# Optimization experiments

Measured on AMD Instinct MI355X. Metric: run time of the kernel, lower is better.

The kernel has to match this reference:

```python
import jax, jax.numpy as jnp
import numpy as np

BINS = 30
MOMENTUM = 0.75
LOSS_WEIGHT = 1.0


def setup_inputs() -> dict:
    key = jax.random.key(0)
    k1, k2 = jax.random.split(key)
    N, C = 8192, 2048
    preds = jax.random.normal(k1, (N, C), dtype=jnp.float32)
    targets = jax.random.randint(k2, (N, C), 0, 2).astype(jnp.int32)  # binary multi-hot
    acc_sum = jnp.zeros((BINS, C), dtype=jnp.float32)  # EMA histogram state
    return {"preds": preds, "targets": targets, "acc_sum": acc_sum}


def reference(preds, targets, acc_sum):
    N, C = preds.shape
    t = targets.astype(preds.dtype)

    # gradient norm g = |sigmoid(p) - t|, detached (weights carry no grad)
    g = jnp.abs(jax.nn.sigmoid(jax.lax.stop_gradient(preds)) - t)

    # bin index: edges[i] = i/BINS, so bin = floor(g*BINS), g=1.0 -> last bin (edge[-1]+=1e-6)
    bin_idx = jnp.clip(jnp.floor(g * BINS).astype(jnp.int32), 0, BINS - 1)  # [N, C]

    # per-label histogram: counts[b, c] = #examples with bin b in column c
    cols = jnp.broadcast_to(jnp.arange(C, dtype=jnp.int32)[None, :], (N, C))
    counts = jnp.zeros((BINS, C), dtype=preds.dtype).at[bin_idx, cols].add(1.0)

    # n[c] = number of non-empty bins for label c
    n = jnp.sum(counts >= 1.0, axis=0).astype(preds.dtype)  # [C]

    # EMA update of the histogram (momentum > 0 branch)
    acc_new = MOMENTUM * acc_sum + (1.0 - MOMENTUM) * counts  # [BINS, C]

    tot = jnp.asarray(float(max(N, 1.0)), preds.dtype)
    weights = tot / acc_new[bin_idx, cols]               # gather per-element density
    weights = weights / jnp.maximum(n, 1.0)[None, :]      # normalize by #valid bins
    weights = jax.lax.stop_gradient(weights)

    # BCE with logits, elementwise: softplus-style stable form
    bce = jnp.logaddexp(0.0, preds) - preds * t
    loss = jnp.mean(weights * bce)
    return loss * LOSS_WEIGHT
```

## Files before the change

### kernel.cpp

```cpp
#include <hip/hip_runtime.h>

#define BINS  30
#define NROWS 8192
#define NCOLS 2048
#define COLS_PER_BLK 256
#define ROWS_PER_BLK 128
#define YSLICES 64

#define FIXED_SCALE 16384.0f
#define CNT_SHIFT   24
#define SUM_MASK    ((1u << CNT_SHIFT) - 1)

#define WS_PART  0
#define WS_CNT   (YSLICES * BINS * NCOLS * 4)
#define WS_BSUM  (WS_CNT + BINS * NCOLS * 4)
#define WS_BPART (WS_BSUM + BINS * NCOLS * 4)

__global__ __launch_bounds__(1024, 8) void k_main(
    const float* __restrict__ preds, const int* __restrict__ targets,
    unsigned int* __restrict__ part)
{
    __shared__ unsigned int h[BINS * COLS_PER_BLK];
    const int tid = threadIdx.x;
    for (int i = tid; i < BINS * COLS_PER_BLK; i += 1024) h[i] = 0u;
    __syncthreads();

    const int wave = tid >> 6;
    const int lane = tid & 63;
    const int colBase = blockIdx.x * COLS_PER_BLK;
    const int col0 = colBase + 4 * lane;
    const int r0   = blockIdx.y * ROWS_PER_BLK + wave * 8;

    const float4* P = (const float4*)(preds   + (size_t)r0 * NCOLS + col0);
    const int4*   T = (const int4*)  (targets + (size_t)r0 * NCOLS + col0);
    const int RV = NCOLS / 4;

    float4 pc0 = P[0], pc1 = P[RV];
    int4   tc0 = T[0], tc1 = T[RV];

    #pragma unroll
    for (int q = 0; q < 4; ++q) {
        float4 pn0, pn1;
        int4   tn0, tn1;
        if (q < 3) {
            P += 2 * RV; T += 2 * RV;
            pn0 = P[0]; pn1 = P[RV];
            tn0 = T[0]; tn1 = T[RV];
        }
        __builtin_amdgcn_sched_barrier(0);

        const float4 pb[2] = {pc0, pc1};
        const int4   tb[2] = {tc0, tc1};
        #pragma unroll
        for (int r = 0; r < 2; ++r) {
            const float pv[4] = {pb[r].x, pb[r].y, pb[r].z, pb[r].w};
            const int   tv[4] = {tb[r].x, tb[r].y, tb[r].z, tb[r].w};
            #pragma unroll
            for (int j = 0; j < 4; ++j) {
                float p  = pv[j];
                float pp = tv[j] ? -p : p;
                float e  = __expf(-fabsf(pp));
                float d  = 1.0f + e;
                float r1 = __builtin_amdgcn_rcpf(d);
                float g  = (pp >= 0.0f) ? r1 : e * r1;
                int   b  = (int)(g * 30.0f);
                b = b > (BINS - 1) ? (BINS - 1) : b;
                float bce = fmaxf(pp, 0.0f) + __logf(d);
                unsigned int pk = (1u << CNT_SHIFT)
                    | (unsigned int)(bce * FIXED_SCALE + 0.5f);
                atomicAdd(&h[b * COLS_PER_BLK + (j << 6) + lane], pk);
            }
        }
        pc0 = pn0; pc1 = pn1;
        tc0 = tn0; tc1 = tn1;
    }
    __syncthreads();

    const size_t outBase = (size_t)blockIdx.y * BINS * NCOLS + colBase;
    for (int i = tid; i < BINS * COLS_PER_BLK; i += 1024) {
        const int b = i >> 8;
        const int r = i & 255;
        const int l = r >> 2;
        const int j = r & 3;
        part[outBase + (size_t)b * NCOLS + r] = h[b * COLS_PER_BLK + (j << 6) + l];
    }
}

__global__ __launch_bounds__(256) void k_reduce(
    const unsigned int* __restrict__ part,
    float* __restrict__ cnt_f, float* __restrict__ bsum_f)
{
    const int id = blockIdx.x * 256 + threadIdx.x;
    unsigned int cnt = 0u, sm = 0u;
    #pragma unroll 16
    for (int y = 0; y < YSLICES; ++y) {
        const unsigned int v = part[(size_t)y * BINS * NCOLS + id];
        cnt += v >> CNT_SHIFT;
        sm  += v & SUM_MASK;
    }
    cnt_f[id]  = (float)cnt;
    bsum_f[id] = (float)sm * (1.0f / FIXED_SCALE);
}

__global__ __launch_bounds__(256) void k_colsum(
    const float* __restrict__ cnt_f, const float* __restrict__ bsum_f,
    const float* __restrict__ acc_sum, float* __restrict__ blockPart)
{
    __shared__ float wave_sums[4];
    const int tid = threadIdx.x;
    const int c   = blockIdx.x * 256 + tid;

    float colsum = 0.0f;
    int n = 0;
    #pragma unroll
    for (int b = 0; b < BINS; ++b) {
        const size_t gidx = (size_t)b * NCOLS + c;
        const float cnt = cnt_f[gidx];
        if (cnt >= 1.0f) {
            n += 1;
            float acc_new = 0.75f * acc_sum[gidx] + 0.25f * cnt;
            colsum += bsum_f[gidx] / acc_new;
        }
    }
    colsum /= (float)((n > 1 ? n : 1) * NCOLS);

    #pragma unroll
    for (int off = 32; off > 0; off >>= 1)
        colsum += __shfl_down(colsum, off, 64);
    if ((tid & 63) == 0) wave_sums[tid >> 6] = colsum;
    __syncthreads();
    if (tid == 0)
        blockPart[blockIdx.x] = wave_sums[0] + wave_sums[1] + wave_sums[2] + wave_sums[3];
}

__global__ void k_final(const float* __restrict__ blockPart, float* __restrict__ out)
{
    double s = 0.0;
    #pragma unroll
    for (int i = 0; i < 8; ++i) s += (double)blockPart[i];
    out[0] = (float)s;
}

extern "C" void kernel_launch(void* const* d_in, const int* in_sizes, int n_in,
                              void* d_out, int out_size, void* d_ws, size_t ws_size,
                              hipStream_t stream)
{
    const float* preds   = (const float*)d_in[0];
    const int*   targets = (const int*)d_in[1];
    const float* acc_sum = (const float*)d_in[2];

    unsigned int* part = (unsigned int*)((char*)d_ws + WS_PART);
    float* cnt_f       = (float*)((char*)d_ws + WS_CNT);
    float* bsum_f      = (float*)((char*)d_ws + WS_BSUM);
    float* blockPart   = (float*)((char*)d_ws + WS_BPART);

    dim3 gA(NCOLS / COLS_PER_BLK, NROWS / ROWS_PER_BLK);
    k_main<<<gA, 1024, 0, stream>>>(preds, targets, part);

    k_reduce<<<(BINS * NCOLS) / 256, 256, 0, stream>>>(part, cnt_f, bsum_f);

    k_colsum<<<NCOLS / 256, 256, 0, stream>>>(cnt_f, bsum_f, acc_sum, blockPart);

    k_final<<<1, 1, 0, stream>>>(blockPart, (float*)d_out);
}
```

Baseline: 179.6 us.

## Replace LDS atomic histogram with per-thread register histograms per column

Each thread now owns a single column and accumulates its 30-bin packed count/sum histogram in registers using unrolled compare-select adds, instead of shared-memory atomics. This removes the LDS atomic traffic and the shared-memory init and flush. The block shape changes to 512 threads covering 512 columns, and the target sign flip becomes an XOR. In exchange it adds 30 VALU ops per element, uses more registers, loads narrower scalar data instead of float4, and launches fewer waves.

```diff
diff --git a/kernel.cpp b/kernel.cpp
--- a/kernel.cpp
+++ b/kernel.cpp
@@ -3,10 +3,8 @@
 #define BINS  30
 #define NROWS 8192
 #define NCOLS 2048
-#define COLS_PER_BLK 256
+#define YSLICES 64
 #define ROWS_PER_BLK 128
-#define YSLICES 64
-
 #define FIXED_SCALE 16384.0f
 #define CNT_SHIFT   24
 #define SUM_MASK    ((1u << CNT_SHIFT) - 1)
@@ -16,74 +14,62 @@
 #define WS_BSUM  (WS_CNT + BINS * NCOLS * 4)
 #define WS_BPART (WS_BSUM + BINS * NCOLS * 4)
 
-__global__ __launch_bounds__(1024, 8) void k_main(
+__device__ __forceinline__ void accum(float p, int t, unsigned int (&h)[BINS])
+{
+    float pp = __int_as_float(__float_as_int(p) ^ (t << 31));
+    float e  = __expf(-fabsf(pp));
+    float d  = 1.0f + e;
+    float r1 = __builtin_amdgcn_rcpf(d);
+    float g  = (pp >= 0.0f) ? r1 : e * r1;
+    int   b  = (int)(g * 30.0f);
+    b = b > (BINS - 1) ? (BINS - 1) : b;
+    float bce = fmaxf(pp, 0.0f) + __logf(d);
+    unsigned int pk = (1u << CNT_SHIFT)
+        | (unsigned int)(bce * FIXED_SCALE + 0.5f);
+    #pragma unroll
+    for (int bb = 0; bb < BINS; ++bb)
+        h[bb] += (b == bb) ? pk : 0u;
+}
+
+__global__ __launch_bounds__(512, 4) void k_main(
     const float* __restrict__ preds, const int* __restrict__ targets,
     unsigned int* __restrict__ part)
 {
-    __shared__ unsigned int h[BINS * COLS_PER_BLK];
     const int tid = threadIdx.x;
-    for (int i = tid; i < BINS * COLS_PER_BLK; i += 1024) h[i] = 0u;
-    __syncthreads();
+    const int col = blockIdx.x * 512 + tid;
+    const int r0  = blockIdx.y * ROWS_PER_BLK;
 
-    const int wave = tid >> 6;
-    const int lane = tid & 63;
-    const int colBase = blockIdx.x * COLS_PER_BLK;
-    const int col0 = colBase + 4 * lane;
-    const int r0   = blockIdx.y * ROWS_PER_BLK + wave * 8;
+    unsigned int h[BINS];
+    #pragma unroll
+    for (int b = 0; b < BINS; ++b) h[b] = 0u;
 
-    const float4* P = (const float4*)(preds   + (size_t)r0 * NCOLS + col0);
-    const int4*   T = (const int4*)  (targets + (size_t)r0 * NCOLS + col0);
-    const int RV = NCOLS / 4;
+    const float* P = preds   + (size_t)r0 * NCOLS + col;
+    const int*   T = targets + (size_t)r0 * NCOLS + col;
 
-    float4 pc0 = P[0], pc1 = P[RV];
-    int4   tc0 = T[0], tc1 = T[RV];
+    float pc[4]; int tc[4];
+    #pragma unroll
+    for (int i = 0; i < 4; ++i) { pc[i] = P[i * NCOLS]; tc[i] = T[i * NCOLS]; }
 
-    #pragma unroll
-    for (int q = 0; q < 4; ++q) {
-        float4 pn0, pn1;
-        int4   tn0, tn1;
-        if (q < 3) {
-            P += 2 * RV; T += 2 * RV;
-            pn0 = P[0]; pn1 = P[RV];
-            tn0 = T[0]; tn1 = T[RV];
+    for (int batch = 0; batch < ROWS_PER_BLK / 4; ++batch) {
+        float pn[4]; int tn[4];
+        if (batch < ROWS_PER_BLK / 4 - 1) {
+            P += 4 * NCOLS; T += 4 * NCOLS;
+            #pragma unroll
+            for (int i = 0; i < 4; ++i) { pn[i] = P[i * NCOLS]; tn[i] = T[i * NCOLS]; }
         }
         __builtin_amdgcn_sched_barrier(0);
 
-        const float4 pb[2] = {pc0, pc1};
-        const int4   tb[2] = {tc0, tc1};
         #pragma unroll
-        for (int r = 0; r < 2; ++r) {
-            const float pv[4] = {pb[r].x, pb[r].y, pb[r].z, pb[r].w};
-            const int   tv[4] = {tb[r].x, tb[r].y, tb[r].z, tb[r].w};
-            #pragma unroll
-            for (int j = 0; j < 4; ++j) {
-                float p  = pv[j];
-                float pp = tv[j] ? -p : p;
-                float e  = __expf(-fabsf(pp));
-                float d  = 1.0f + e;
-                float r1 = __builtin_amdgcn_rcpf(d);
-                float g  = (pp >= 0.0f) ? r1 : e * r1;
-                int   b  = (int)(g * 30.0f);
-                b = b > (BINS - 1) ? (BINS - 1) : b;
-                float bce = fmaxf(pp, 0.0f) + __logf(d);
-                unsigned int pk = (1u << CNT_SHIFT)
-                    | (unsigned int)(bce * FIXED_SCALE + 0.5f);
-                atomicAdd(&h[b * COLS_PER_BLK + (j << 6) + lane], pk);
-            }
-        }
-        pc0 = pn0; pc1 = pn1;
-        tc0 = tn0; tc1 = tn1;
+        for (int i = 0; i < 4; ++i) accum(pc[i], tc[i], h);
+
+        #pragma unroll
+        for (int i = 0; i < 4; ++i) { pc[i] = pn[i]; tc[i] = tn[i]; }
     }
-    __syncthreads();
 
-    const size_t outBase = (size_t)blockIdx.y * BINS * NCOLS + colBase;
-    for (int i = tid; i < BINS * COLS_PER_BLK; i += 1024) {
-        const int b = i >> 8;
-        const int r = i & 255;
-        const int l = r >> 2;
-        const int j = r & 3;
-        part[outBase + (size_t)b * NCOLS + r] = h[b * COLS_PER_BLK + (j << 6) + l];
-    }
+    unsigned int* base = part + (size_t)blockIdx.y * BINS * NCOLS + col;
+    #pragma unroll
+    for (int b = 0; b < BINS; ++b)
+        base[(size_t)b * NCOLS] = h[b];
 }
 
 __global__ __launch_bounds__(256) void k_reduce(
@@ -154,8 +140,8 @@
     float* bsum_f      = (float*)((char*)d_ws + WS_BSUM);
     float* blockPart   = (float*)((char*)d_ws + WS_BPART);
 
-    dim3 gA(NCOLS / COLS_PER_BLK, NROWS / ROWS_PER_BLK);
-    k_main<<<gA, 1024, 0, stream>>>(preds, targets, part);
+    dim3 gA(NCOLS / 512, YSLICES);
+    k_main<<<gA, 512, 0, stream>>>(preds, targets, part);
 
     k_reduce<<<(BINS * NCOLS) / 256, 256, 0, stream>>>(part, cnt_f, bsum_f);
 
```

Measured after the change: 209.4 us. +16.6%, slower.
